# Performance work log

Measured on AMD Instinct MI355X. Metric: run time of the kernel, lower is better.

The kernel has to match this reference:

```python
import jax, jax.numpy as jnp
import numpy as np

E = 1_000_000   # metapath instances (edges)
N = 100_000     # destination nodes
H = 8           # num_heads
D = 32          # out_dim
NUM_ETYPES = 3
ALPHA = 0.01    # leaky relu slope
ETYPES = [0, 1, 2]  # etypes_mapping is identity


def setup_inputs() -> dict:
    key = jax.random.key(0)
    k = jax.random.split(key, 6)
    # xavier_normal gain=1.414 for attn: std = gain*sqrt(2/(fan_in+fan_out))
    attn_std = 1.414 * np.sqrt(2.0 / (1 + D))
    return {
        "feat0": jax.random.normal(k[0], (E, D), jnp.float32),
        "feat1": jax.random.normal(k[1], (E, D), jnp.float32),
        "feat2": jax.random.normal(k[2], (E, D), jnp.float32),
        "r_vec": jax.random.normal(k[3], (NUM_ETYPES, D), jnp.float32),
        "attn": jax.random.normal(k[4], (1, H, D), jnp.float32) * attn_std,
        "dst": jax.random.randint(k[5], (E,), 0, N, dtype=jnp.int32),
        "num_nodes": N,
    }


def _l2norm(x):
    # torch F.normalize(p=2, dim=1)
    return x / jnp.maximum(jnp.linalg.norm(x, axis=1, keepdims=True), 1e-12)


def reference(feat0, feat1, feat2, r_vec, attn, dst, num_nodes):
    # --- TransE1 metapath-instance encoding ---
    feats = [_l2norm(feat0), _l2norm(feat1), _l2norm(feat2)]
    for i in range(len(ETYPES) - 1):
        feats[i] = feats[i] + r_vec[jnp.asarray(ETYPES[i:])].sum(axis=0)
    hidden = (feats[0] + feats[1] + feats[2]) / 3.0           # [E, D]
    # cat H copies then view(-1, H, D) == broadcast over head dim
    eft = jnp.broadcast_to(hidden[:, None, :], (hidden.shape[0], H, D))  # [E, H, D]

    # --- per-edge attention logits ---
    a = jnp.sum(eft * attn, axis=-1, keepdims=True)           # [E, H, 1]
    a = jax.nn.leaky_relu(a, negative_slope=ALPHA)

    # --- segment (edge) softmax over destination nodes ---
    m = jax.ops.segment_max(a, dst, num_segments=num_nodes)   # [N, H, 1]
    ex = jnp.exp(a - m[dst])
    s = jax.ops.segment_sum(ex, dst, num_segments=num_nodes)  # [N, H, 1]
    att = ex / s[dst]                                         # [E, H, 1]

    # --- weighted scatter-sum aggregation ---
    out = jax.ops.segment_sum(eft * att, dst, num_segments=num_nodes)  # [N, H, D]
    return out
```

## Files before the change

kernel.cpp:

```cpp
#include <hip/hip_runtime.h>
#include <hip/hip_fp16.h>

#define DD 32
#define HH 8
#define CAP 64
#define ALPHA 0.01f

__global__ __launch_bounds__(256) void k_init(int* __restrict__ cnt, int N) {
    int i = blockIdx.x * 256 + threadIdx.x;
    if (i < N) cnt[i] = 0;
}

__global__ __launch_bounds__(256) void k_edge(
    const float* __restrict__ f0, const float* __restrict__ f1, const float* __restrict__ f2,
    const float* __restrict__ rv, const float* __restrict__ attn,
    const int* __restrict__ dst, int E,
    __half* __restrict__ hidden, float* __restrict__ exa,
    int* __restrict__ cnt, int* __restrict__ slots)
{
    __shared__ float4 s_attn[HH * 8];
    __shared__ float s_R[DD];
    int t = threadIdx.x;
    if (t < 64) s_attn[t] = ((const float4*)attn)[t];
    if (t >= 64 && t < 96) {
        int d = t - 64;
        s_R[d] = rv[d] + 2.0f * (rv[DD + d] + rv[2 * DD + d]);
    }
    __syncthreads();

    int e = blockIdx.x * 256 + t;
    if (e >= E) return;

    int n = dst[e];
    int r = atomicAdd(&cnt[n], 1);

    union HU { float4 v4[8]; float s[DD]; } h;

    {
        const float4* p = (const float4*)(f0 + (size_t)e * DD);
        float4 v[8]; float ss = 0.0f;
        #pragma unroll
        for (int i = 0; i < 8; i++) { v[i] = p[i];
            ss += v[i].x*v[i].x + v[i].y*v[i].y + v[i].z*v[i].z + v[i].w*v[i].w; }
        float inv = 1.0f / fmaxf(sqrtf(ss), 1e-12f);
        #pragma unroll
        for (int i = 0; i < 8; i++)
            h.v4[i] = make_float4(v[i].x*inv, v[i].y*inv, v[i].z*inv, v[i].w*inv);
    }
    {
        const float4* p = (const float4*)(f1 + (size_t)e * DD);
        float4 v[8]; float ss = 0.0f;
        #pragma unroll
        for (int i = 0; i < 8; i++) { v[i] = p[i];
            ss += v[i].x*v[i].x + v[i].y*v[i].y + v[i].z*v[i].z + v[i].w*v[i].w; }
        float inv = 1.0f / fmaxf(sqrtf(ss), 1e-12f);
        #pragma unroll
        for (int i = 0; i < 8; i++) {
            h.v4[i].x += v[i].x*inv; h.v4[i].y += v[i].y*inv;
            h.v4[i].z += v[i].z*inv; h.v4[i].w += v[i].w*inv; }
    }
    {
        const float4* p = (const float4*)(f2 + (size_t)e * DD);
        float4 v[8]; float ss = 0.0f;
        #pragma unroll
        for (int i = 0; i < 8; i++) { v[i] = p[i];
            ss += v[i].x*v[i].x + v[i].y*v[i].y + v[i].z*v[i].z + v[i].w*v[i].w; }
        float inv = 1.0f / fmaxf(sqrtf(ss), 1e-12f);
        #pragma unroll
        for (int i = 0; i < 8; i++) {
            h.v4[i].x += v[i].x*inv; h.v4[i].y += v[i].y*inv;
            h.v4[i].z += v[i].z*inv; h.v4[i].w += v[i].w*inv; }
    }
    #pragma unroll
    for (int d = 0; d < DD; d++) h.s[d] = (h.s[d] + s_R[d]) * (1.0f / 3.0f);

    {
        union { __half2 h2[16]; float4 f4[4]; } u;
        #pragma unroll
        for (int i = 0; i < 16; i++) u.h2[i] = __floats2half2_rn(h.s[2*i], h.s[2*i+1]);
        float4* hp = (float4*)(hidden + (size_t)e * DD);
        #pragma unroll
        for (int i = 0; i < 4; i++) hp[i] = u.f4[i];
    }

    float ex[HH];
    #pragma unroll
    for (int q = 0; q < HH; q++) {
        float acc = 0.0f;
        #pragma unroll
        for (int i = 0; i < 8; i++) {
            float4 w = s_attn[q * 8 + i];
            float4 x = h.v4[i];
            acc += x.x*w.x + x.y*w.y + x.z*w.z + x.w*w.w;
        }
        float a = acc > 0.0f ? acc : ALPHA * acc;
        ex[q] = __expf(a);
    }
    float4* ap = (float4*)(exa + (size_t)e * HH);
    ap[0] = make_float4(ex[0], ex[1], ex[2], ex[3]);
    ap[1] = make_float4(ex[4], ex[5], ex[6], ex[7]);

    if (r < CAP) slots[(size_t)n * CAP + r] = e;
}

__global__ __launch_bounds__(256) void k_agg(
    const __half* __restrict__ hidden, const float* __restrict__ exa,
    const int* __restrict__ cnt, const int* __restrict__ slots,
    const int* __restrict__ dst, float* __restrict__ out, int N, int E)
{
    int wid = threadIdx.x >> 6, lane = threadIdx.x & 63;
    int n = blockIdx.x * 4 + wid;
    if (n >= N) return;
    int degraw = cnt[n];
    int d = lane & 31;
    int hq = lane >> 5;
    float ssum[4] = {0.f, 0.f, 0.f, 0.f};
    float acc[4]  = {0.f, 0.f, 0.f, 0.f};

    if (degraw <= CAP) {
        int deg = degraw;
        int ev = (lane < deg) ? slots[(size_t)n * CAP + lane] : 0;
        int j = 0;
        for (; j + 1 < deg; j += 2) {
            int ea = __shfl(ev, j), eb = __shfl(ev, j + 1);
            float4 xa = *(const float4*)(exa + (size_t)ea * HH + hq * 4);
            float  ha = __half2float(hidden[(size_t)ea * DD + d]);
            float4 xb = *(const float4*)(exa + (size_t)eb * HH + hq * 4);
            float  hb = __half2float(hidden[(size_t)eb * DD + d]);
            ssum[0] += xa.x; ssum[1] += xa.y; ssum[2] += xa.z; ssum[3] += xa.w;
            acc[0] += xa.x * ha; acc[1] += xa.y * ha; acc[2] += xa.z * ha; acc[3] += xa.w * ha;
            ssum[0] += xb.x; ssum[1] += xb.y; ssum[2] += xb.z; ssum[3] += xb.w;
            acc[0] += xb.x * hb; acc[1] += xb.y * hb; acc[2] += xb.z * hb; acc[3] += xb.w * hb;
        }
        if (j < deg) {
            int ea = __shfl(ev, j);
            float4 xa = *(const float4*)(exa + (size_t)ea * HH + hq * 4);
            float  ha = __half2float(hidden[(size_t)ea * DD + d]);
            ssum[0] += xa.x; ssum[1] += xa.y; ssum[2] += xa.z; ssum[3] += xa.w;
            acc[0] += xa.x * ha; acc[1] += xa.y * ha; acc[2] += xa.z * ha; acc[3] += xa.w * ha;
        }
    } else {
        for (int base = 0; base < E; base += 64) {
            int e = base + lane;
            bool mt = (e < E) && (dst[e] == n);
            unsigned long long mk = __ballot(mt);
            while (mk) {
                int l = __ffsll(mk) - 1; mk &= mk - 1;
                int em = base + l;
                float4 x = *(const float4*)(exa + (size_t)em * HH + hq * 4);
                float  hd = __half2float(hidden[(size_t)em * DD + d]);
                ssum[0] += x.x; ssum[1] += x.y; ssum[2] += x.z; ssum[3] += x.w;
                acc[0] += x.x * hd; acc[1] += x.y * hd; acc[2] += x.z * hd; acc[3] += x.w * hd;
            }
        }
    }

    size_t ob = (size_t)n * (HH * DD) + hq * 128 + d;
    #pragma unroll
    for (int k = 0; k < 4; k++) {
        float sv = ssum[k];
        float rr = sv > 0.0f ? 1.0f / sv : 0.0f;
        out[ob + k * 32] = acc[k] * rr;
    }
}

extern "C" void kernel_launch(void* const* d_in, const int* in_sizes, int n_in,
                              void* d_out, int out_size, void* d_ws, size_t ws_size,
                              hipStream_t stream)
{
    const float* f0   = (const float*)d_in[0];
    const float* f1   = (const float*)d_in[1];
    const float* f2   = (const float*)d_in[2];
    const float* rv   = (const float*)d_in[3];
    const float* attn = (const float*)d_in[4];
    const int*   dst  = (const int*)d_in[5];
    int E = in_sizes[0] / DD;
    int N = out_size / (HH * DD);
    float* out = (float*)d_out;

    auto al = [](size_t x) { return (x + 255) & ~(size_t)255; };
    char* w = (char*)d_ws;
    size_t off = 0;
    __half* hidden = (__half*)(w + off); off += al((size_t)E * DD * 2);
    float*  exa    = (float*)(w + off);  off += al((size_t)E * HH * 4);
    int*    cnt    = (int*)(w + off);    off += al((size_t)N * 4);
    int*    slots  = (int*)(w + off);    off += al((size_t)N * CAP * 4);
    (void)ws_size; (void)n_in;

    k_init<<<(N + 255) / 256, 256, 0, stream>>>(cnt, N);

    int gridE = (E + 255) / 256;
    k_edge<<<gridE, 256, 0, stream>>>(f0, f1, f2, rv, attn, dst, E, hidden, exa, cnt, slots);

    int gridN = (N + 3) / 4;
    k_agg<<<gridN, 256, 0, stream>>>(hidden, exa, cnt, slots, dst, out, N, E);
}
```

Baseline: 508.9 us.

## Build CSR via count+scan and write per-edge records grouped by destination

Replaces the fixed-capacity slot table with a count pass, a three-kernel prefix scan building row pointers, and a scatter of per-edge records (exp logits plus half hidden) into destination-sorted order. Aggregation then reads contiguous records per node instead of gathering by edge index, and the fallback full-scan path for high-degree nodes is removed. It also loads all three feature rows up front for more memory-level parallelism. The cost is extra launches, an extra pass over dst, and scattered writes in the edge kernel.

```diff
diff --git a/kernel.cpp b/kernel.cpp
--- a/kernel.cpp
+++ b/kernel.cpp
@@ -3,20 +3,87 @@
 
 #define DD 32
 #define HH 8
-#define CAP 64
 #define ALPHA 0.01f
-
-__global__ __launch_bounds__(256) void k_init(int* __restrict__ cnt, int N) {
+#define REC 24
+#define SCAN_T 256
+#define SCAN_E 1024
+
+__global__ __launch_bounds__(256) void k_zero(int* __restrict__ cnt, int N) {
     int i = blockIdx.x * 256 + threadIdx.x;
     if (i < N) cnt[i] = 0;
+}
+
+__global__ __launch_bounds__(256) void k_count(const int* __restrict__ dst, int E,
+                                               int* __restrict__ cnt) {
+    int e = blockIdx.x * 256 + threadIdx.x;
+    if (e < E) atomicAdd(&cnt[dst[e]], 1);
+}
+
+__global__ __launch_bounds__(SCAN_T) void k_scan1(const int* __restrict__ cnt, int N,
+                                                  int* __restrict__ bsum) {
+    __shared__ int sh[SCAN_T];
+    int t = threadIdx.x, b = blockIdx.x;
+    int base = b * SCAN_E + t * 4;
+    int s = 0;
+    #pragma unroll
+    for (int k = 0; k < 4; k++) { int i = base + k; if (i < N) s += cnt[i]; }
+    sh[t] = s; __syncthreads();
+    for (int off = SCAN_T / 2; off > 0; off >>= 1) {
+        if (t < off) sh[t] += sh[t + off];
+        __syncthreads();
+    }
+    if (t == 0) bsum[b] = sh[0];
+}
+
+__global__ __launch_bounds__(SCAN_T) void k_scan2(const int* __restrict__ bsum, int nb,
+                                                  int* __restrict__ boff) {
+    __shared__ int sh[SCAN_T];
+    int t = threadIdx.x;
+    int x = (t < nb) ? bsum[t] : 0;
+    sh[t] = x; __syncthreads();
+    for (int off = 1; off < SCAN_T; off <<= 1) {
+        int v = (t >= off) ? sh[t - off] : 0;
+        __syncthreads();
+        sh[t] += v;
+        __syncthreads();
+    }
+    if (t < nb) boff[t] = sh[t] - x;
+}
+
+__global__ __launch_bounds__(SCAN_T) void k_scan3(const int* __restrict__ cnt, int N, int E,
+                                                  const int* __restrict__ boff,
+                                                  int* __restrict__ row_ptr) {
+    __shared__ int sh[SCAN_T];
+    int t = threadIdx.x, b = blockIdx.x;
+    int base = b * SCAN_E + t * 4;
+    int c[4];
+    #pragma unroll
+    for (int k = 0; k < 4; k++) { int i = base + k; c[k] = (i < N) ? cnt[i] : 0; }
+    int ts = c[0] + c[1] + c[2] + c[3];
+    sh[t] = ts; __syncthreads();
+    for (int off = 1; off < SCAN_T; off <<= 1) {
+        int v = (t >= off) ? sh[t - off] : 0;
+        __syncthreads();
+        sh[t] += v;
+        __syncthreads();
+    }
+    int rp = boff[b] + sh[t] - ts;
+    int acc = 0;
+    #pragma unroll
+    for (int k = 0; k < 4; k++) {
+        int i = base + k;
+        if (i < N) row_ptr[i] = rp + acc;
+        acc += c[k];
+    }
+    if (b == 0 && t == 0) row_ptr[N] = E;
 }
 
 __global__ __launch_bounds__(256) void k_edge(
     const float* __restrict__ f0, const float* __restrict__ f1, const float* __restrict__ f2,
     const float* __restrict__ rv, const float* __restrict__ attn,
     const int* __restrict__ dst, int E,
-    __half* __restrict__ hidden, float* __restrict__ exa,
-    int* __restrict__ cnt, int* __restrict__ slots)
+    const int* __restrict__ row_ptr, int* __restrict__ cnt,
+    float* __restrict__ records)
 {
     __shared__ float4 s_attn[HH * 8];
     __shared__ float s_R[DD];
@@ -32,55 +99,38 @@
     if (e >= E) return;
 
     int n = dst[e];
-    int r = atomicAdd(&cnt[n], 1);
+    int rp0 = row_ptr[n];
+    int r = atomicAdd(&cnt[n], -1) - 1;
+
+    const float4* p0 = (const float4*)(f0 + (size_t)e * DD);
+    const float4* p1 = (const float4*)(f1 + (size_t)e * DD);
+    const float4* p2 = (const float4*)(f2 + (size_t)e * DD);
+    float4 a0[8], a1[8], a2[8];
+    #pragma unroll
+    for (int i = 0; i < 8; i++) a0[i] = p0[i];
+    #pragma unroll
+    for (int i = 0; i < 8; i++) a1[i] = p1[i];
+    #pragma unroll
+    for (int i = 0; i < 8; i++) a2[i] = p2[i];
+
+    float s0 = 0.f, s1 = 0.f, s2 = 0.f;
+    #pragma unroll
+    for (int i = 0; i < 8; i++) {
+        s0 += a0[i].x*a0[i].x + a0[i].y*a0[i].y + a0[i].z*a0[i].z + a0[i].w*a0[i].w;
+        s1 += a1[i].x*a1[i].x + a1[i].y*a1[i].y + a1[i].z*a1[i].z + a1[i].w*a1[i].w;
+        s2 += a2[i].x*a2[i].x + a2[i].y*a2[i].y + a2[i].z*a2[i].z + a2[i].w*a2[i].w;
+    }
+    float i0 = 1.0f / fmaxf(sqrtf(s0), 1e-12f);
+    float i1 = 1.0f / fmaxf(sqrtf(s1), 1e-12f);
+    float i2 = 1.0f / fmaxf(sqrtf(s2), 1e-12f);
 
     union HU { float4 v4[8]; float s[DD]; } h;
-
-    {
-        const float4* p = (const float4*)(f0 + (size_t)e * DD);
-        float4 v[8]; float ss = 0.0f;
-        #pragma unroll
-        for (int i = 0; i < 8; i++) { v[i] = p[i];
-            ss += v[i].x*v[i].x + v[i].y*v[i].y + v[i].z*v[i].z + v[i].w*v[i].w; }
-        float inv = 1.0f / fmaxf(sqrtf(ss), 1e-12f);
-        #pragma unroll
-        for (int i = 0; i < 8; i++)
-            h.v4[i] = make_float4(v[i].x*inv, v[i].y*inv, v[i].z*inv, v[i].w*inv);
-    }
-    {
-        const float4* p = (const float4*)(f1 + (size_t)e * DD);
-        float4 v[8]; float ss = 0.0f;
-        #pragma unroll
-        for (int i = 0; i < 8; i++) { v[i] = p[i];
-            ss += v[i].x*v[i].x + v[i].y*v[i].y + v[i].z*v[i].z + v[i].w*v[i].w; }
-        float inv = 1.0f / fmaxf(sqrtf(ss), 1e-12f);
-        #pragma unroll
-        for (int i = 0; i < 8; i++) {
-            h.v4[i].x += v[i].x*inv; h.v4[i].y += v[i].y*inv;
-            h.v4[i].z += v[i].z*inv; h.v4[i].w += v[i].w*inv; }
-    }
-    {
-        const float4* p = (const float4*)(f2 + (size_t)e * DD);
-        float4 v[8]; float ss = 0.0f;
-        #pragma unroll
-        for (int i = 0; i < 8; i++) { v[i] = p[i];
-            ss += v[i].x*v[i].x + v[i].y*v[i].y + v[i].z*v[i].z + v[i].w*v[i].w; }
-        float inv = 1.0f / fmaxf(sqrtf(ss), 1e-12f);
-        #pragma unroll
-        for (int i = 0; i < 8; i++) {
-            h.v4[i].x += v[i].x*inv; h.v4[i].y += v[i].y*inv;
-            h.v4[i].z += v[i].z*inv; h.v4[i].w += v[i].w*inv; }
-    }
-    #pragma unroll
-    for (int d = 0; d < DD; d++) h.s[d] = (h.s[d] + s_R[d]) * (1.0f / 3.0f);
-
-    {
-        union { __half2 h2[16]; float4 f4[4]; } u;
-        #pragma unroll
-        for (int i = 0; i < 16; i++) u.h2[i] = __floats2half2_rn(h.s[2*i], h.s[2*i+1]);
-        float4* hp = (float4*)(hidden + (size_t)e * DD);
-        #pragma unroll
-        for (int i = 0; i < 4; i++) hp[i] = u.f4[i];
+    #pragma unroll
+    for (int i = 0; i < 8; i++) {
+        h.v4[i].x = (a0[i].x*i0 + a1[i].x*i1 + a2[i].x*i2 + s_R[4*i+0]) * (1.0f/3.0f);
+        h.v4[i].y = (a0[i].y*i0 + a1[i].y*i1 + a2[i].y*i2 + s_R[4*i+1]) * (1.0f/3.0f);
+        h.v4[i].z = (a0[i].z*i0 + a1[i].z*i1 + a2[i].z*i2 + s_R[4*i+2]) * (1.0f/3.0f);
+        h.v4[i].w = (a0[i].w*i0 + a1[i].w*i1 + a2[i].w*i2 + s_R[4*i+3]) * (1.0f/3.0f);
     }
 
     float ex[HH];
@@ -96,63 +146,54 @@
         float a = acc > 0.0f ? acc : ALPHA * acc;
         ex[q] = __expf(a);
     }
-    float4* ap = (float4*)(exa + (size_t)e * HH);
-    ap[0] = make_float4(ex[0], ex[1], ex[2], ex[3]);
-    ap[1] = make_float4(ex[4], ex[5], ex[6], ex[7]);
-
-    if (r < CAP) slots[(size_t)n * CAP + r] = e;
+
+    union PU { __half2 h2[16]; float4 f4[4]; } u;
+    #pragma unroll
+    for (int i = 0; i < 16; i++) u.h2[i] = __floats2half2_rn(h.s[2*i], h.s[2*i+1]);
+
+    float* recp = records + (size_t)(rp0 + r) * REC;
+    float4* rq = (float4*)recp;
+    rq[0] = make_float4(ex[0], ex[1], ex[2], ex[3]);
+    rq[1] = make_float4(ex[4], ex[5], ex[6], ex[7]);
+    #pragma unroll
+    for (int i = 0; i < 4; i++) rq[2 + i] = u.f4[i];
 }
 
 __global__ __launch_bounds__(256) void k_agg(
-    const __half* __restrict__ hidden, const float* __restrict__ exa,
-    const int* __restrict__ cnt, const int* __restrict__ slots,
-    const int* __restrict__ dst, float* __restrict__ out, int N, int E)
+    const float* __restrict__ records, const int* __restrict__ row_ptr,
+    float* __restrict__ out, int N)
 {
     int wid = threadIdx.x >> 6, lane = threadIdx.x & 63;
     int n = blockIdx.x * 4 + wid;
     if (n >= N) return;
-    int degraw = cnt[n];
+    int r0 = row_ptr[n], r1 = row_ptr[n + 1];
+    int deg = r1 - r0;
     int d = lane & 31;
     int hq = lane >> 5;
+
     float ssum[4] = {0.f, 0.f, 0.f, 0.f};
     float acc[4]  = {0.f, 0.f, 0.f, 0.f};
-
-    if (degraw <= CAP) {
-        int deg = degraw;
-        int ev = (lane < deg) ? slots[(size_t)n * CAP + lane] : 0;
-        int j = 0;
-        for (; j + 1 < deg; j += 2) {
-            int ea = __shfl(ev, j), eb = __shfl(ev, j + 1);
-            float4 xa = *(const float4*)(exa + (size_t)ea * HH + hq * 4);
-            float  ha = __half2float(hidden[(size_t)ea * DD + d]);
-            float4 xb = *(const float4*)(exa + (size_t)eb * HH + hq * 4);
-            float  hb = __half2float(hidden[(size_t)eb * DD + d]);
-            ssum[0] += xa.x; ssum[1] += xa.y; ssum[2] += xa.z; ssum[3] += xa.w;
-            acc[0] += xa.x * ha; acc[1] += xa.y * ha; acc[2] += xa.z * ha; acc[3] += xa.w * ha;
-            ssum[0] += xb.x; ssum[1] += xb.y; ssum[2] += xb.z; ssum[3] += xb.w;
-            acc[0] += xb.x * hb; acc[1] += xb.y * hb; acc[2] += xb.z * hb; acc[3] += xb.w * hb;
-        }
-        if (j < deg) {
-            int ea = __shfl(ev, j);
-            float4 xa = *(const float4*)(exa + (size_t)ea * HH + hq * 4);
-            float  ha = __half2float(hidden[(size_t)ea * DD + d]);
-            ssum[0] += xa.x; ssum[1] += xa.y; ssum[2] += xa.z; ssum[3] += xa.w;
-            acc[0] += xa.x * ha; acc[1] += xa.y * ha; acc[2] += xa.z * ha; acc[3] += xa.w * ha;
-        }
-    } else {
-        for (int base = 0; base < E; base += 64) {
-            int e = base + lane;
-            bool mt = (e < E) && (dst[e] == n);
-            unsigned long long mk = __ballot(mt);
-            while (mk) {
-                int l = __ffsll(mk) - 1; mk &= mk - 1;
-                int em = base + l;
-                float4 x = *(const float4*)(exa + (size_t)em * HH + hq * 4);
-                float  hd = __half2float(hidden[(size_t)em * DD + d]);
-                ssum[0] += x.x; ssum[1] += x.y; ssum[2] += x.z; ssum[3] += x.w;
-                acc[0] += x.x * hd; acc[1] += x.y * hd; acc[2] += x.z * hd; acc[3] += x.w * hd;
-            }
-        }
+    const float* rec = records + (size_t)r0 * REC;
+
+    int j = 0;
+    for (; j + 1 < deg; j += 2) {
+        const float* ra = rec + (size_t)j * REC;
+        const float* rb = ra + REC;
+        float4 xa = *(const float4*)(ra + hq * 4);
+        float  ha = __half2float(((const __half*)(ra + 8))[d]);
+        float4 xb = *(const float4*)(rb + hq * 4);
+        float  hb = __half2float(((const __half*)(rb + 8))[d]);
+        ssum[0] += xa.x; ssum[1] += xa.y; ssum[2] += xa.z; ssum[3] += xa.w;
+        acc[0] += xa.x * ha; acc[1] += xa.y * ha; acc[2] += xa.z * ha; acc[3] += xa.w * ha;
+        ssum[0] += xb.x; ssum[1] += xb.y; ssum[2] += xb.z; ssum[3] += xb.w;
+        acc[0] += xb.x * hb; acc[1] += xb.y * hb; acc[2] += xb.z * hb; acc[3] += xb.w * hb;
+    }
+    if (j < deg) {
+        const float* ra = rec + (size_t)j * REC;
+        float4 xa = *(const float4*)(ra + hq * 4);
+        float  ha = __half2float(((const __half*)(ra + 8))[d]);
+        ssum[0] += xa.x; ssum[1] += xa.y; ssum[2] += xa.z; ssum[3] += xa.w;
+        acc[0] += xa.x * ha; acc[1] += xa.y * ha; acc[2] += xa.z * ha; acc[3] += xa.w * ha;
     }
 
     size_t ob = (size_t)n * (HH * DD) + hq * 128 + d;
@@ -181,17 +222,21 @@
     auto al = [](size_t x) { return (x + 255) & ~(size_t)255; };
     char* w = (char*)d_ws;
     size_t off = 0;
-    __half* hidden = (__half*)(w + off); off += al((size_t)E * DD * 2);
-    float*  exa    = (float*)(w + off);  off += al((size_t)E * HH * 4);
-    int*    cnt    = (int*)(w + off);    off += al((size_t)N * 4);
-    int*    slots  = (int*)(w + off);    off += al((size_t)N * CAP * 4);
+    float* records = (float*)(w + off); off += al((size_t)E * REC * 4);
+    int* row_ptr   = (int*)(w + off);   off += al(((size_t)N + 1) * 4);
+    int* cnt       = (int*)(w + off);   off += al((size_t)N * 4);
+    int* bsum      = (int*)(w + off);   off += al((size_t)SCAN_T * 4);
+    int* boff      = (int*)(w + off);   off += al((size_t)SCAN_T * 4);
     (void)ws_size; (void)n_in;
 
-    k_init<<<(N + 255) / 256, 256, 0, stream>>>(cnt, N);
-
+    int nb = (N + SCAN_E - 1) / SCAN_E;
+
+    k_zero<<<(N + 255) / 256, 256, 0, stream>>>(cnt, N);
     int gridE = (E + 255) / 256;
-    k_edge<<<gridE, 256, 0, stream>>>(f0, f1, f2, rv, attn, dst, E, hidden, exa, cnt, slots);
-
-    int gridN = (N + 3) / 4;
-    k_agg<<<gridN, 256, 0, stream>>>(hidden, exa, cnt, slots, dst, out, N, E);
-}
+    k_count<<<gridE, 256, 0, stream>>>(dst, E, cnt);
+    k_scan1<<<nb, SCAN_T, 0, stream>>>(cnt, N, bsum);
+    k_scan2<<<1, SCAN_T, 0, stream>>>(bsum, nb, boff);
+    k_scan3<<<nb, SCAN_T, 0, stream>>>(cnt, N, E, boff, row_ptr);
+    k_edge<<<gridE, 256, 0, stream>>>(f0, f1, f2, rv, attn, dst, E, row_ptr, cnt, records);
+    k_agg<<<(N + 3) / 4, 256, 0, stream>>>(records, row_ptr, out, N);
+}
```

Result: slower. 563.0 us (+10.6%).

## Fuse edge encoding into node-grouped aggregation with LDS staging and overflow list

Applied to the files above, without the earlier changes.

Splits slot assignment into its own kernel, then fuses per-edge TransE encoding and attention-logit computation into the aggregation kernel. Each block handles 16 nodes, encodes their gathered edges into shared memory, and reduces them there, so the intermediate hidden/exp arrays are never written to or read back from global memory. Nodes with more than 32 edges send the extra edges to a global overflow list that the owning block scans. In exchange, feature rows are read through gathered indices instead of streamed, shared-memory use is large, and the overflow path is a serial scan.

```diff
diff --git a/kernel.cpp b/kernel.cpp
--- a/kernel.cpp
+++ b/kernel.cpp
@@ -1,166 +1,244 @@
 #include <hip/hip_runtime.h>
-#include <hip/hip_fp16.h>
 
 #define DD 32
 #define HH 8
-#define CAP 64
 #define ALPHA 0.01f
-
-__global__ __launch_bounds__(256) void k_init(int* __restrict__ cnt, int N) {
+#define CAP 32
+#define G 16
+#define ECH 256
+#define LST 44
+#define OVF_MAX (1 << 20)
+
+__global__ __launch_bounds__(256) void k_zero(int* __restrict__ cnt, int* __restrict__ ovfc, int N) {
     int i = blockIdx.x * 256 + threadIdx.x;
     if (i < N) cnt[i] = 0;
-}
-
-__global__ __launch_bounds__(256) void k_edge(
+    if (i == 0) *ovfc = 0;
+}
+
+__global__ __launch_bounds__(256) void k_slot(const int* __restrict__ dst, int E,
+                                              int* __restrict__ cnt, int* __restrict__ slots,
+                                              int* __restrict__ ovfc, int2* __restrict__ ovf) {
+    int e = blockIdx.x * 256 + threadIdx.x;
+    if (e >= E) return;
+    int n = dst[e];
+    int r = atomicAdd(&cnt[n], 1);
+    if (r < CAP) slots[(size_t)n * CAP + r] = e;
+    else { int k = atomicAdd(ovfc, 1); if (k < OVF_MAX) ovf[k] = make_int2(e, n); }
+}
+
+__device__ __noinline__ void ovf_encode(const float* __restrict__ f0, const float* __restrict__ f1,
+                                        const float* __restrict__ f2, const float* __restrict__ s_R,
+                                        const float* __restrict__ s_att, int e, int d,
+                                        float* hd, float* ex) {
+    float h[DD];
+    float s0 = 0.f, s1 = 0.f, s2 = 0.f;
+    for (int i = 0; i < DD; i++) {
+        float x0 = f0[(size_t)e * DD + i], x1 = f1[(size_t)e * DD + i], x2 = f2[(size_t)e * DD + i];
+        s0 += x0 * x0; s1 += x1 * x1; s2 += x2 * x2;
+        h[i] = x0;
+    }
+    float i0 = 1.0f / fmaxf(sqrtf(s0), 1e-12f);
+    float i1 = 1.0f / fmaxf(sqrtf(s1), 1e-12f);
+    float i2 = 1.0f / fmaxf(sqrtf(s2), 1e-12f);
+    for (int i = 0; i < DD; i++) {
+        float x1 = f1[(size_t)e * DD + i], x2 = f2[(size_t)e * DD + i];
+        h[i] = (h[i] * i0 + x1 * i1 + x2 * i2 + s_R[i]) * (1.0f / 3.0f);
+    }
+    for (int q = 0; q < HH; q++) {
+        float a = 0.f;
+        for (int i = 0; i < DD; i++) a += h[i] * s_att[q * DD + i];
+        a = a > 0.f ? a : ALPHA * a;
+        ex[q] = __expf(a);
+    }
+    *hd = h[d];
+}
+
+__global__ __launch_bounds__(256) void k_fused(
     const float* __restrict__ f0, const float* __restrict__ f1, const float* __restrict__ f2,
     const float* __restrict__ rv, const float* __restrict__ attn,
-    const int* __restrict__ dst, int E,
-    __half* __restrict__ hidden, float* __restrict__ exa,
-    int* __restrict__ cnt, int* __restrict__ slots)
+    const int* __restrict__ slots, const int* __restrict__ cnt,
+    const int* __restrict__ ovfc, const int2* __restrict__ ovf,
+    float* __restrict__ out, int N)
 {
-    __shared__ float4 s_attn[HH * 8];
+    __shared__ float s_att[HH * DD];
     __shared__ float s_R[DD];
+    __shared__ float s_edge[ECH * LST];
+    __shared__ int s_p[G + 1];
+    __shared__ int s_rawdeg[G];
+
     int t = threadIdx.x;
-    if (t < 64) s_attn[t] = ((const float4*)attn)[t];
-    if (t >= 64 && t < 96) {
-        int d = t - 64;
-        s_R[d] = rv[d] + 2.0f * (rv[DD + d] + rv[2 * DD + d]);
+    s_att[t] = attn[t];
+    if (t < DD) s_R[t] = rv[t] + 2.0f * (rv[DD + t] + rv[2 * DD + t]);
+    int b0 = blockIdx.x * G;
+    if (t < G) {
+        int n = b0 + t;
+        s_rawdeg[t] = (n < N) ? cnt[n] : 0;
     }
     __syncthreads();
-
-    int e = blockIdx.x * 256 + t;
-    if (e >= E) return;
-
-    int n = dst[e];
-    int r = atomicAdd(&cnt[n], 1);
-
-    union HU { float4 v4[8]; float s[DD]; } h;
-
-    {
-        const float4* p = (const float4*)(f0 + (size_t)e * DD);
-        float4 v[8]; float ss = 0.0f;
+    if (t == 0) {
+        int a = 0;
+        for (int i = 0; i < G; i++) {
+            s_p[i] = a;
+            int dg = s_rawdeg[i];
+            a += (dg < CAP ? dg : CAP);
+        }
+        s_p[G] = a;
+    }
+    __syncthreads();
+    int total = s_p[G];
+
+    int d = t & 31, nl0 = t >> 5;
+    float num0[HH], den0[HH], num1[HH], den1[HH];
+    #pragma unroll
+    for (int q = 0; q < HH; q++) { num0[q] = den0[q] = num1[q] = den1[q] = 0.f; }
+
+    for (int base = 0; base < total; base += ECH) {
+        int idx = base + t;
+        if (idx < total) {
+            int nl = 0;
+            if (idx >= s_p[nl + 8]) nl += 8;
+            if (idx >= s_p[nl + 4]) nl += 4;
+            if (idx >= s_p[nl + 2]) nl += 2;
+            if (idx >= s_p[nl + 1]) nl += 1;
+            int j = idx - s_p[nl];
+            int e = slots[(size_t)(b0 + nl) * CAP + j];
+
+            const float4* p0 = (const float4*)(f0 + (size_t)e * DD);
+            const float4* p1 = (const float4*)(f1 + (size_t)e * DD);
+            const float4* p2 = (const float4*)(f2 + (size_t)e * DD);
+            float4 hv[8];
+            {
+                float4 v[8]; float ss = 0.f;
+                #pragma unroll
+                for (int i = 0; i < 8; i++) { v[i] = p0[i];
+                    ss += v[i].x*v[i].x + v[i].y*v[i].y + v[i].z*v[i].z + v[i].w*v[i].w; }
+                float inv = 1.0f / fmaxf(sqrtf(ss), 1e-12f);
+                #pragma unroll
+                for (int i = 0; i < 8; i++)
+                    hv[i] = make_float4(v[i].x*inv, v[i].y*inv, v[i].z*inv, v[i].w*inv);
+            }
+            {
+                float4 v[8]; float ss = 0.f;
+                #pragma unroll
+                for (int i = 0; i < 8; i++) { v[i] = p1[i];
+                    ss += v[i].x*v[i].x + v[i].y*v[i].y + v[i].z*v[i].z + v[i].w*v[i].w; }
+                float inv = 1.0f / fmaxf(sqrtf(ss), 1e-12f);
+                #pragma unroll
+                for (int i = 0; i < 8; i++) {
+                    hv[i].x += v[i].x*inv; hv[i].y += v[i].y*inv;
+                    hv[i].z += v[i].z*inv; hv[i].w += v[i].w*inv; }
+            }
+            {
+                float4 v[8]; float ss = 0.f;
+                #pragma unroll
+                for (int i = 0; i < 8; i++) { v[i] = p2[i];
+                    ss += v[i].x*v[i].x + v[i].y*v[i].y + v[i].z*v[i].z + v[i].w*v[i].w; }
+                float inv = 1.0f / fmaxf(sqrtf(ss), 1e-12f);
+                #pragma unroll
+                for (int i = 0; i < 8; i++) {
+                    hv[i].x += v[i].x*inv; hv[i].y += v[i].y*inv;
+                    hv[i].z += v[i].z*inv; hv[i].w += v[i].w*inv; }
+            }
+            const float4* R4 = (const float4*)s_R;
+            #pragma unroll
+            for (int i = 0; i < 8; i++) {
+                float4 r = R4[i];
+                hv[i].x = (hv[i].x + r.x) * (1.0f/3.0f);
+                hv[i].y = (hv[i].y + r.y) * (1.0f/3.0f);
+                hv[i].z = (hv[i].z + r.z) * (1.0f/3.0f);
+                hv[i].w = (hv[i].w + r.w) * (1.0f/3.0f);
+            }
+            float ex[HH];
+            const float4* A4 = (const float4*)s_att;
+            #pragma unroll
+            for (int q = 0; q < HH; q++) {
+                float a = 0.f;
+                #pragma unroll
+                for (int i = 0; i < 8; i++) {
+                    float4 w = A4[q * 8 + i];
+                    a += hv[i].x*w.x + hv[i].y*w.y + hv[i].z*w.z + hv[i].w*w.w;
+                }
+                a = a > 0.f ? a : ALPHA * a;
+                ex[q] = __expf(a);
+            }
+            float* sl = &s_edge[t * LST];
+            float4* sl4 = (float4*)sl;
+            #pragma unroll
+            for (int i = 0; i < 8; i++) sl4[i] = hv[i];
+            sl4[8] = make_float4(ex[0], ex[1], ex[2], ex[3]);
+            sl4[9] = make_float4(ex[4], ex[5], ex[6], ex[7]);
+        }
+        __syncthreads();
+
+        {
+            int a0 = s_p[nl0] - base, a1 = s_p[nl0 + 1] - base;
+            if (a0 < 0) a0 = 0;
+            if (a1 > ECH) a1 = ECH;
+            for (int s = a0; s < a1; s++) {
+                const float* sp = &s_edge[s * LST];
+                float h = sp[d];
+                #pragma unroll
+                for (int q = 0; q < HH; q++) { float x = sp[32 + q]; den0[q] += x; num0[q] += x * h; }
+            }
+        }
+        {
+            int a0 = s_p[nl0 + 8] - base, a1 = s_p[nl0 + 9] - base;
+            if (a0 < 0) a0 = 0;
+            if (a1 > ECH) a1 = ECH;
+            for (int s = a0; s < a1; s++) {
+                const float* sp = &s_edge[s * LST];
+                float h = sp[d];
+                #pragma unroll
+                for (int q = 0; q < HH; q++) { float x = sp[32 + q]; den1[q] += x; num1[q] += x * h; }
+            }
+        }
+        __syncthreads();
+    }
+
+    int novf = *ovfc;
+    if (novf > OVF_MAX) novf = OVF_MAX;
+    if (novf > 0) {
+        int nA = b0 + nl0;
+        if (nA < N && s_rawdeg[nl0] > CAP) {
+            for (int k = 0; k < novf; k++) {
+                int2 pr = ovf[k];
+                if (pr.y != nA) continue;
+                float hd, ex[HH];
+                ovf_encode(f0, f1, f2, s_R, s_att, pr.x, d, &hd, ex);
+                #pragma unroll
+                for (int q = 0; q < HH; q++) { den0[q] += ex[q]; num0[q] += ex[q] * hd; }
+            }
+        }
+        int nB = b0 + nl0 + 8;
+        if (nB < N && s_rawdeg[nl0 + 8] > CAP) {
+            for (int k = 0; k < novf; k++) {
+                int2 pr = ovf[k];
+                if (pr.y != nB) continue;
+                float hd, ex[HH];
+                ovf_encode(f0, f1, f2, s_R, s_att, pr.x, d, &hd, ex);
+                #pragma unroll
+                for (int q = 0; q < HH; q++) { den1[q] += ex[q]; num1[q] += ex[q] * hd; }
+            }
+        }
+    }
+
+    int nA = b0 + nl0;
+    if (nA < N) {
+        size_t ob = (size_t)nA * (HH * DD) + d;
         #pragma unroll
-        for (int i = 0; i < 8; i++) { v[i] = p[i];
-            ss += v[i].x*v[i].x + v[i].y*v[i].y + v[i].z*v[i].z + v[i].w*v[i].w; }
-        float inv = 1.0f / fmaxf(sqrtf(ss), 1e-12f);
+        for (int q = 0; q < HH; q++) {
+            float dv = den0[q];
+            out[ob + q * DD] = dv > 0.f ? num0[q] / dv : 0.f;
+        }
+    }
+    int nB = b0 + nl0 + 8;
+    if (nB < N) {
+        size_t ob = (size_t)nB * (HH * DD) + d;
         #pragma unroll
-        for (int i = 0; i < 8; i++)
-            h.v4[i] = make_float4(v[i].x*inv, v[i].y*inv, v[i].z*inv, v[i].w*inv);
-    }
-    {
-        const float4* p = (const float4*)(f1 + (size_t)e * DD);
-        float4 v[8]; float ss = 0.0f;
-        #pragma unroll
-        for (int i = 0; i < 8; i++) { v[i] = p[i];
-            ss += v[i].x*v[i].x + v[i].y*v[i].y + v[i].z*v[i].z + v[i].w*v[i].w; }
-        float inv = 1.0f / fmaxf(sqrtf(ss), 1e-12f);
-        #pragma unroll
-        for (int i = 0; i < 8; i++) {
-            h.v4[i].x += v[i].x*inv; h.v4[i].y += v[i].y*inv;
-            h.v4[i].z += v[i].z*inv; h.v4[i].w += v[i].w*inv; }
-    }
-    {
-        const float4* p = (const float4*)(f2 + (size_t)e * DD);
-        float4 v[8]; float ss = 0.0f;
-        #pragma unroll
-        for (int i = 0; i < 8; i++) { v[i] = p[i];
-            ss += v[i].x*v[i].x + v[i].y*v[i].y + v[i].z*v[i].z + v[i].w*v[i].w; }
-        float inv = 1.0f / fmaxf(sqrtf(ss), 1e-12f);
-        #pragma unroll
-        for (int i = 0; i < 8; i++) {
-            h.v4[i].x += v[i].x*inv; h.v4[i].y += v[i].y*inv;
-            h.v4[i].z += v[i].z*inv; h.v4[i].w += v[i].w*inv; }
-    }
-    #pragma unroll
-    for (int d = 0; d < DD; d++) h.s[d] = (h.s[d] + s_R[d]) * (1.0f / 3.0f);
-
-    {
-        union { __half2 h2[16]; float4 f4[4]; } u;
-        #pragma unroll
-        for (int i = 0; i < 16; i++) u.h2[i] = __floats2half2_rn(h.s[2*i], h.s[2*i+1]);
-        float4* hp = (float4*)(hidden + (size_t)e * DD);
-        #pragma unroll
-        for (int i = 0; i < 4; i++) hp[i] = u.f4[i];
-    }
-
-    float ex[HH];
-    #pragma unroll
-    for (int q = 0; q < HH; q++) {
-        float acc = 0.0f;
-        #pragma unroll
-        for (int i = 0; i < 8; i++) {
-            float4 w = s_attn[q * 8 + i];
-            float4 x = h.v4[i];
-            acc += x.x*w.x + x.y*w.y + x.z*w.z + x.w*w.w;
-        }
-        float a = acc > 0.0f ? acc : ALPHA * acc;
-        ex[q] = __expf(a);
-    }
-    float4* ap = (float4*)(exa + (size_t)e * HH);
-    ap[0] = make_float4(ex[0], ex[1], ex[2], ex[3]);
-    ap[1] = make_float4(ex[4], ex[5], ex[6], ex[7]);
-
-    if (r < CAP) slots[(size_t)n * CAP + r] = e;
-}
-
-__global__ __launch_bounds__(256) void k_agg(
-    const __half* __restrict__ hidden, const float* __restrict__ exa,
-    const int* __restrict__ cnt, const int* __restrict__ slots,
-    const int* __restrict__ dst, float* __restrict__ out, int N, int E)
-{
-    int wid = threadIdx.x >> 6, lane = threadIdx.x & 63;
-    int n = blockIdx.x * 4 + wid;
-    if (n >= N) return;
-    int degraw = cnt[n];
-    int d = lane & 31;
-    int hq = lane >> 5;
-    float ssum[4] = {0.f, 0.f, 0.f, 0.f};
-    float acc[4]  = {0.f, 0.f, 0.f, 0.f};
-
-    if (degraw <= CAP) {
-        int deg = degraw;
-        int ev = (lane < deg) ? slots[(size_t)n * CAP + lane] : 0;
-        int j = 0;
-        for (; j + 1 < deg; j += 2) {
-            int ea = __shfl(ev, j), eb = __shfl(ev, j + 1);
-            float4 xa = *(const float4*)(exa + (size_t)ea * HH + hq * 4);
-            float  ha = __half2float(hidden[(size_t)ea * DD + d]);
-            float4 xb = *(const float4*)(exa + (size_t)eb * HH + hq * 4);
-            float  hb = __half2float(hidden[(size_t)eb * DD + d]);
-            ssum[0] += xa.x; ssum[1] += xa.y; ssum[2] += xa.z; ssum[3] += xa.w;
-            acc[0] += xa.x * ha; acc[1] += xa.y * ha; acc[2] += xa.z * ha; acc[3] += xa.w * ha;
-            ssum[0] += xb.x; ssum[1] += xb.y; ssum[2] += xb.z; ssum[3] += xb.w;
-            acc[0] += xb.x * hb; acc[1] += xb.y * hb; acc[2] += xb.z * hb; acc[3] += xb.w * hb;
-        }
-        if (j < deg) {
-            int ea = __shfl(ev, j);
-            float4 xa = *(const float4*)(exa + (size_t)ea * HH + hq * 4);
-            float  ha = __half2float(hidden[(size_t)ea * DD + d]);
-            ssum[0] += xa.x; ssum[1] += xa.y; ssum[2] += xa.z; ssum[3] += xa.w;
-            acc[0] += xa.x * ha; acc[1] += xa.y * ha; acc[2] += xa.z * ha; acc[3] += xa.w * ha;
-        }
-    } else {
-        for (int base = 0; base < E; base += 64) {
-            int e = base + lane;
-            bool mt = (e < E) && (dst[e] == n);
-            unsigned long long mk = __ballot(mt);
-            while (mk) {
-                int l = __ffsll(mk) - 1; mk &= mk - 1;
-                int em = base + l;
-                float4 x = *(const float4*)(exa + (size_t)em * HH + hq * 4);
-                float  hd = __half2float(hidden[(size_t)em * DD + d]);
-                ssum[0] += x.x; ssum[1] += x.y; ssum[2] += x.z; ssum[3] += x.w;
-                acc[0] += x.x * hd; acc[1] += x.y * hd; acc[2] += x.z * hd; acc[3] += x.w * hd;
-            }
-        }
-    }
-
-    size_t ob = (size_t)n * (HH * DD) + hq * 128 + d;
-    #pragma unroll
-    for (int k = 0; k < 4; k++) {
-        float sv = ssum[k];
-        float rr = sv > 0.0f ? 1.0f / sv : 0.0f;
-        out[ob + k * 32] = acc[k] * rr;
+        for (int q = 0; q < HH; q++) {
+            float dv = den1[q];
+            out[ob + q * DD] = dv > 0.f ? num1[q] / dv : 0.f;
+        }
     }
 }
 
@@ -181,17 +259,14 @@
     auto al = [](size_t x) { return (x + 255) & ~(size_t)255; };
     char* w = (char*)d_ws;
     size_t off = 0;
-    __half* hidden = (__half*)(w + off); off += al((size_t)E * DD * 2);
-    float*  exa    = (float*)(w + off);  off += al((size_t)E * HH * 4);
-    int*    cnt    = (int*)(w + off);    off += al((size_t)N * 4);
-    int*    slots  = (int*)(w + off);    off += al((size_t)N * CAP * 4);
+    int*  slots = (int*)(w + off);  off += al((size_t)N * CAP * 4);
+    int*  cnt   = (int*)(w + off);  off += al((size_t)N * 4);
+    int*  ovfc  = (int*)(w + off);  off += al(256);
+    int2* ovf   = (int2*)(w + off); off += al((size_t)OVF_MAX * 8);
     (void)ws_size; (void)n_in;
 
-    k_init<<<(N + 255) / 256, 256, 0, stream>>>(cnt, N);
-
-    int gridE = (E + 255) / 256;
-    k_edge<<<gridE, 256, 0, stream>>>(f0, f1, f2, rv, attn, dst, E, hidden, exa, cnt, slots);
-
-    int gridN = (N + 3) / 4;
-    k_agg<<<gridN, 256, 0, stream>>>(hidden, exa, cnt, slots, dst, out, N, E);
-}
+    k_zero<<<(N + 255) / 256, 256, 0, stream>>>(cnt, ovfc, N);
+    k_slot<<<(E + 255) / 256, 256, 0, stream>>>(dst, E, cnt, slots, ovfc, ovf);
+    k_fused<<<(N + G - 1) / G, 256, 0, stream>>>(f0, f1, f2, rv, attn, slots, cnt,
+                                                 ovfc, ovf, out, N);
+}
```

New measurement: 524.7 us. +3.1%, slower.
